# Kernel optimization log

Hardware: AMD Instinct MI355X
Metric: run time of the kernel (lower is better)

The kernel has to match this reference:

```python
import jax, jax.numpy as jnp
import numpy as np

B, T, C = 4, 2048, 1024

def setup_inputs() -> dict:
    key = jax.random.key(0)
    kx, kq, kk, kv = jax.random.split(key, 4)
    s = C ** -0.5  # match nn.Linear init scale roughly
    return {
        "x": jax.random.normal(kx, (B, T, C), dtype=jnp.float32),
        "Wq": jax.random.normal(kq, (C, C), dtype=jnp.float32) * s,
        "Wk": jax.random.normal(kk, (C, C), dtype=jnp.float32) * s,
        "Wv": jax.random.normal(kv, (C, C), dtype=jnp.float32) * s,
    }

def reference(x, Wq, Wk, Wv):
    Bq, Tq, Cq = x.shape
    # nn.Linear: y = x @ W^T (bias=False)
    q = jnp.einsum('btc,dc->btd', x, Wq)
    k = jnp.einsum('btc,dc->btd', x, Wk)
    v = jnp.einsum('btc,dc->btd', x, Wv)
    scale = Cq ** -0.5
    qk = jnp.einsum('btd,bsd->bts', q, k) * scale  # [B, T, T]
    causal = jnp.tril(jnp.ones((Tq, Tq), dtype=bool))
    qk = jnp.where(causal, qk, -jnp.inf)
    attn = jax.nn.softmax(qk, axis=-1)
    out = jnp.einsum('bts,bsd->btd', attn, v)
    return out
```

## Files before the change

### kernel.cpp

```cpp
#include <hip/hip_runtime.h>
#include <hip/hip_fp16.h>


typedef __attribute__((ext_vector_type(8))) _Float16 half8;
typedef __attribute__((ext_vector_type(4))) _Float16 half4;
typedef __attribute__((ext_vector_type(4))) float f32x4;

#define AS1 __attribute__((address_space(1)))
#define AS3 __attribute__((address_space(3)))

__device__ __forceinline__ void gload_lds16(const void* g, void* l) {
    __builtin_amdgcn_global_load_lds((AS1 void*)g, (AS3 void*)l, 16, 0, 0);
}

__device__ __forceinline__ void barrier_np() {
    __asm__ volatile("" ::: "memory");
    __builtin_amdgcn_s_barrier();
    __asm__ volatile("" ::: "memory");
}

template<int TM, int TN, bool SWAP>
__device__ __forceinline__ void gemm_nt_dbuf(
    const _Float16* __restrict__ A, const _Float16* __restrict__ B,
    int lda, int ldb, int k0, int k1,
    _Float16* ldsA, _Float16* ldsB,
    f32x4 acc[TM / 32][TN / 32])
{
    constexpr int FM = TM / 32, FN = TN / 32;
    constexpr int NA = TM / 64, NB = TN / 64;
    constexpr int WAIT_IMM = 0xF70 | (NA + NB);
    const int t    = threadIdx.x;
    const int lane = t & 63;
    const int wm   = (t >> 7) & 1;
    const int wn   = (t >> 6) & 1;
    const int lr   = lane & 15;
    const int lq   = lane >> 4;

    const _Float16* ga[NA]; int loA[NA];
    const _Float16* gb[NB]; int loB[NB];
#pragma unroll
    for (int i = 0; i < NA; ++i) {
        int f = t + 256 * i;
        int r = f >> 2, c = ((f & 3) ^ ((f >> 3) & 3)) * 8;
        ga[i] = A + (size_t)r * lda + c;
        loA[i] = f * 8;
    }
#pragma unroll
    for (int i = 0; i < NB; ++i) {
        int f = t + 256 * i;
        int r = f >> 2, c = ((f & 3) ^ ((f >> 3) & 3)) * 8;
        gb[i] = B + (size_t)r * ldb + c;
        loB[i] = f * 8;
    }

    int offA[FM], offB[FN];
#pragma unroll
    for (int i = 0; i < FM; ++i) {
        int R = wm * (TM / 2) + i * 16 + lr;
        offA[i] = (R * 4 + ((lq ^ (R >> 1)) & 3)) * 8;
    }
#pragma unroll
    for (int i = 0; i < FN; ++i) {
        int R = wn * (TN / 2) + i * 16 + lr;
        offB[i] = (R * 4 + ((lq ^ (R >> 1)) & 3)) * 8;
    }

#pragma unroll
    for (int i = 0; i < NA; ++i) gload_lds16(ga[i] + k0, ldsA + loA[i]);
#pragma unroll
    for (int i = 0; i < NB; ++i) gload_lds16(gb[i] + k0, ldsB + loB[i]);

    int sel = 0;
    for (int k = k0; k < k1; k += 32) {
        const int kp = (k + 32 < k1) ? k + 32 : k;
        _Float16* pA = ldsA + (sel ^ 1) * (TM * 32);
        _Float16* pB = ldsB + (sel ^ 1) * (TN * 32);
#pragma unroll
        for (int i = 0; i < NA; ++i) gload_lds16(ga[i] + kp, pA + loA[i]);
#pragma unroll
        for (int i = 0; i < NB; ++i) gload_lds16(gb[i] + kp, pB + loB[i]);

        __builtin_amdgcn_s_waitcnt(WAIT_IMM);
        barrier_np();

        const _Float16* bufA = ldsA + sel * (TM * 32);
        const _Float16* bufB = ldsB + sel * (TN * 32);
        half8 af[FM], bf[FN];
#pragma unroll
        for (int i = 0; i < FM; ++i) af[i] = *(const half8*)(bufA + offA[i]);
#pragma unroll
        for (int i = 0; i < FN; ++i) bf[i] = *(const half8*)(bufB + offB[i]);
#pragma unroll
        for (int mi = 0; mi < FM; ++mi)
#pragma unroll
            for (int ni = 0; ni < FN; ++ni) {
                if constexpr (SWAP)
                    acc[mi][ni] = __builtin_amdgcn_mfma_f32_16x16x32_f16(
                        bf[ni], af[mi], acc[mi][ni], 0, 0, 0);
                else
                    acc[mi][ni] = __builtin_amdgcn_mfma_f32_16x16x32_f16(
                        af[mi], bf[ni], acc[mi][ni], 0, 0, 0);
            }
        barrier_np();
        sel ^= 1;
    }
}

__global__ __launch_bounds__(256) void f32tof16_k(
    const float* __restrict__ in, _Float16* __restrict__ out, int n)
{
    int i = (blockIdx.x * 256 + threadIdx.x) * 4;
    if (i < n) {
        float4 f = *(const float4*)(in + i);
        half4 h = { (_Float16)f.x, (_Float16)f.y, (_Float16)f.z, (_Float16)f.w };
        *(half4*)(out + i) = h;
    }
}

__global__ __launch_bounds__(256) void wconv_k(
    const float* __restrict__ Wq, const float* __restrict__ Wk,
    const float* __restrict__ Wv, _Float16* __restrict__ out)
{
    const float* src = (blockIdx.y == 0) ? Wq : (blockIdx.y == 1) ? Wk : Wv;
    int i = (blockIdx.x * 256 + threadIdx.x) * 4;
    float4 f = *(const float4*)(src + i);
    half4 h = { (_Float16)f.x, (_Float16)f.y, (_Float16)f.z, (_Float16)f.w };
    *(half4*)(out + (size_t)blockIdx.y * 1024 * 1024 + i) = h;
}

__global__ __launch_bounds__(256) void qkv_gemm_k(
    const _Float16* __restrict__ xh, const _Float16* __restrict__ Wh,
    _Float16* __restrict__ Q, _Float16* __restrict__ K, _Float16* __restrict__ Vt)
{
    __shared__ __align__(16) _Float16 ldsA[2 * 128 * 32];
    __shared__ __align__(16) _Float16 ldsB[2 * 128 * 32];
    const int tileM = blockIdx.x * 128;
    const int tileN = blockIdx.y * 128;
    const int z     = blockIdx.z;
    const _Float16* W = Wh + (size_t)z * 1024 * 1024;

    const int lane = threadIdx.x & 63;
    const int wm = (threadIdx.x >> 7) & 1, wn = (threadIdx.x >> 6) & 1;
    const int lr = lane & 15, lq = lane >> 4;

    if (z == 2) {
        f32x4 acc[4][4] = {};
        gemm_nt_dbuf<128, 128, false>(xh + (size_t)tileM * 1024,
                                      W + (size_t)tileN * 1024,
                                      1024, 1024, 0, 1024, ldsA, ldsB, acc);
#pragma unroll
        for (int mi = 0; mi < 4; ++mi)
#pragma unroll
            for (int ni = 0; ni < 4; ++ni) {
                int m0 = tileM + wm * 64 + mi * 16 + lq * 4;
                int n  = tileN + wn * 64 + ni * 16 + lr;
                int b = m0 >> 11, tt = m0 & 2047;
                half4 h = { (_Float16)acc[mi][ni][0], (_Float16)acc[mi][ni][1],
                            (_Float16)acc[mi][ni][2], (_Float16)acc[mi][ni][3] };
                *(half4*)(Vt + (size_t)b * 2048 * 1024 + (size_t)n * 2048 + tt) = h;
            }
    } else {
        f32x4 acc[4][4] = {};
        gemm_nt_dbuf<128, 128, true>(xh + (size_t)tileM * 1024,
                                     W + (size_t)tileN * 1024,
                                     1024, 1024, 0, 1024, ldsA, ldsB, acc);
        _Float16* O = (z == 0) ? Q : K;
#pragma unroll
        for (int mi = 0; mi < 4; ++mi)
#pragma unroll
            for (int ni = 0; ni < 4; ++ni) {
                int tt = tileM + wm * 64 + mi * 16 + lr;
                int d0 = tileN + wn * 64 + ni * 16 + lq * 4;
                half4 h = { (_Float16)acc[mi][ni][0], (_Float16)acc[mi][ni][1],
                            (_Float16)acc[mi][ni][2], (_Float16)acc[mi][ni][3] };
                *(half4*)(O + (size_t)tt * 1024 + d0) = h;
            }
    }
}

__global__ __launch_bounds__(256) void scores_gemm_k(
    const _Float16* __restrict__ Q, const _Float16* __restrict__ K,
    _Float16* __restrict__ S)
{
    const int ti = blockIdx.x, si = blockIdx.y;
    if (si > ti) return;
    const int tileT = ti * 128, tileS = si * 128, b = blockIdx.z;

    __shared__ __align__(16) _Float16 ldsA[2 * 128 * 32];
    __shared__ __align__(16) _Float16 ldsB[2 * 128 * 32];
    f32x4 acc[4][4] = {};
    gemm_nt_dbuf<128, 128, true>(
        Q + (size_t)b * 2048 * 1024 + (size_t)tileT * 1024,
        K + (size_t)b * 2048 * 1024 + (size_t)tileS * 1024,
        1024, 1024, 0, 1024, ldsA, ldsB, acc);

    const int lane = threadIdx.x & 63;
    const int wm = (threadIdx.x >> 7) & 1, wn = (threadIdx.x >> 6) & 1;
    const int lr = lane & 15, lq = lane >> 4;
    const float scale = 0.03125f;

#pragma unroll
    for (int mi = 0; mi < 4; ++mi)
#pragma unroll
        for (int ni = 0; ni < 4; ++ni) {
            int tt = tileT + wm * 64 + mi * 16 + lr;
            int s0 = tileS + wn * 64 + ni * 16 + lq * 4;
            half4 h;
#pragma unroll
            for (int r = 0; r < 4; ++r)
                h[r] = (s0 + r <= tt) ? (_Float16)(acc[mi][ni][r] * scale)
                                      : (_Float16)0.f;
            *(half4*)(S + ((size_t)b * 2048 + tt) * 2048 + s0) = h;
        }
}

__global__ __launch_bounds__(256) void softmax_k(_Float16* __restrict__ S)
{
    const int w    = threadIdx.x >> 6;
    const int lane = threadIdx.x & 63;
    const int t    = blockIdx.x * 4 + w;
    const int b    = blockIdx.y;
    _Float16* row = S + ((size_t)b * 2048 + t) * 2048;

    float x[32];
    float mx = -1e30f;
#pragma unroll
    for (int j = 0; j < 4; ++j) {
        half8 h = *(const half8*)(row + j * 512 + lane * 8);
#pragma unroll
        for (int e = 0; e < 8; ++e) {
            int s = j * 512 + lane * 8 + e;
            float f = (s <= t) ? (float)h[e] : -1e30f;
            x[j * 8 + e] = f;
            mx = fmaxf(mx, f);
        }
    }
#pragma unroll
    for (int o = 32; o > 0; o >>= 1) mx = fmaxf(mx, __shfl_xor(mx, o));

    float sum = 0.f;
#pragma unroll
    for (int i = 0; i < 32; ++i) {
        float e = __expf(x[i] - mx);
        x[i] = e;
        sum += e;
    }
#pragma unroll
    for (int o = 32; o > 0; o >>= 1) sum += __shfl_xor(sum, o);
    const float inv = 1.0f / sum;

#pragma unroll
    for (int j = 0; j < 4; ++j) {
        half8 p;
#pragma unroll
        for (int e = 0; e < 8; ++e) p[e] = (_Float16)(x[j * 8 + e] * inv);
        *(half8*)(row + j * 512 + lane * 8) = p;
    }
}

__global__ __launch_bounds__(256) void pv_gemm_k(
    const _Float16* __restrict__ P, const _Float16* __restrict__ Vt,
    float* __restrict__ out)
{
    __shared__ __align__(16) _Float16 ldsA[2 * 128 * 32];
    __shared__ __align__(16) _Float16 ldsB[2 * 64 * 32];
    const int tileT = (15 - blockIdx.x) * 128;
    const int tileD = blockIdx.y * 64;
    const int b     = blockIdx.z;
    const int kEnd  = tileT + 128;

    f32x4 acc[4][2] = {};
    gemm_nt_dbuf<128, 64, true>(
        P + ((size_t)b * 2048 + tileT) * 2048,
        Vt + (size_t)b * 1024 * 2048 + (size_t)tileD * 2048,
        2048, 2048, 0, kEnd, ldsA, ldsB, acc);

    const int lane = threadIdx.x & 63;
    const int wm = (threadIdx.x >> 7) & 1, wn = (threadIdx.x >> 6) & 1;
    const int lr = lane & 15, lq = lane >> 4;

#pragma unroll
    for (int mi = 0; mi < 4; ++mi)
#pragma unroll
        for (int ni = 0; ni < 2; ++ni) {
            int tt = tileT + wm * 64 + mi * 16 + lr;
            int d0 = tileD + wn * 32 + ni * 16 + lq * 4;
            *(f32x4*)(out + ((size_t)b * 2048 + tt) * 1024 + d0) = acc[mi][ni];
        }
}

extern "C" void kernel_launch(void* const* d_in, const int* in_sizes, int n_in,
                              void* d_out, int out_size, void* d_ws, size_t ws_size,
                              hipStream_t stream)
{
    const float* x  = (const float*)d_in[0];
    const float* Wq = (const float*)d_in[1];
    const float* Wk = (const float*)d_in[2];
    const float* Wv = (const float*)d_in[3];
    float* out = (float*)d_out;

    char* ws = (char*)d_ws;
    _Float16* xh = (_Float16*)(ws);
    _Float16* Wh = (_Float16*)(ws + (16u << 20));
    _Float16* Qh = (_Float16*)(ws + (22u << 20));
    _Float16* Kh = (_Float16*)(ws + (38u << 20));
    _Float16* Vt = (_Float16*)(ws + (54u << 20));
    _Float16* S  = (_Float16*)(ws + (70u << 20));

    f32tof16_k<<<8192, 256, 0, stream>>>(x, xh, 4 * 2048 * 1024);
    wconv_k<<<dim3(1024, 3), 256, 0, stream>>>(Wq, Wk, Wv, Wh);

    qkv_gemm_k<<<dim3(64, 8, 3), 256, 0, stream>>>(xh, Wh, Qh, Kh, Vt);

    scores_gemm_k<<<dim3(16, 16, 4), 256, 0, stream>>>(Qh, Kh, S);
    softmax_k<<<dim3(512, 4), 256, 0, stream>>>(S);
    pv_gemm_k<<<dim3(16, 16, 4), 256, 0, stream>>>(S, Vt, out);
}
```

Baseline: 284.8 us.

## Replace double-buffered BK=32 GEMM loop with single-buffered BK=64 loop

The shared GEMM core drops the double-buffered K=32 pipeline, where the next tile's global-to-LDS loads overlapped the MFMAs, and uses a single buffer with a K step of 64 and two syncthreads per iteration. The LDS swizzle changes to an 8-chunk XOR pattern to fit the wider rows. This halves the number of loop iterations and barriers, but each iteration now waits for its own loads to land before computing, so load latency is no longer hidden within a block. Whether performance holds depends on occupancy across blocks covering that latency.

```diff
diff --git a/kernel.cpp b/kernel.cpp
--- a/kernel.cpp
+++ b/kernel.cpp
@@ -13,22 +13,15 @@
     __builtin_amdgcn_global_load_lds((AS1 void*)g, (AS3 void*)l, 16, 0, 0);
 }
 
-__device__ __forceinline__ void barrier_np() {
-    __asm__ volatile("" ::: "memory");
-    __builtin_amdgcn_s_barrier();
-    __asm__ volatile("" ::: "memory");
-}
-
 template<int TM, int TN, bool SWAP>
-__device__ __forceinline__ void gemm_nt_dbuf(
+__device__ __forceinline__ void gemm_nt_core(
     const _Float16* __restrict__ A, const _Float16* __restrict__ B,
     int lda, int ldb, int k0, int k1,
     _Float16* ldsA, _Float16* ldsB,
     f32x4 acc[TM / 32][TN / 32])
 {
     constexpr int FM = TM / 32, FN = TN / 32;
-    constexpr int NA = TM / 64, NB = TN / 64;
-    constexpr int WAIT_IMM = 0xF70 | (NA + NB);
+    constexpr int NA = TM / 32, NB = TN / 32;
     const int t    = threadIdx.x;
     const int lane = t & 63;
     const int wm   = (t >> 7) & 1;
@@ -41,68 +34,60 @@
 #pragma unroll
     for (int i = 0; i < NA; ++i) {
         int f = t + 256 * i;
-        int r = f >> 2, c = ((f & 3) ^ ((f >> 3) & 3)) * 8;
-        ga[i] = A + (size_t)r * lda + c;
+        int r = f >> 3, c = (f & 7) ^ ((f >> 3) & 7);
+        ga[i] = A + (size_t)r * lda + c * 8;
         loA[i] = f * 8;
     }
 #pragma unroll
     for (int i = 0; i < NB; ++i) {
         int f = t + 256 * i;
-        int r = f >> 2, c = ((f & 3) ^ ((f >> 3) & 3)) * 8;
-        gb[i] = B + (size_t)r * ldb + c;
+        int r = f >> 3, c = (f & 7) ^ ((f >> 3) & 7);
+        gb[i] = B + (size_t)r * ldb + c * 8;
         loB[i] = f * 8;
     }
 
-    int offA[FM], offB[FN];
-#pragma unroll
-    for (int i = 0; i < FM; ++i) {
-        int R = wm * (TM / 2) + i * 16 + lr;
-        offA[i] = (R * 4 + ((lq ^ (R >> 1)) & 3)) * 8;
-    }
-#pragma unroll
-    for (int i = 0; i < FN; ++i) {
-        int R = wn * (TN / 2) + i * 16 + lr;
-        offB[i] = (R * 4 + ((lq ^ (R >> 1)) & 3)) * 8;
-    }
-
-#pragma unroll
-    for (int i = 0; i < NA; ++i) gload_lds16(ga[i] + k0, ldsA + loA[i]);
-#pragma unroll
-    for (int i = 0; i < NB; ++i) gload_lds16(gb[i] + k0, ldsB + loB[i]);
-
-    int sel = 0;
-    for (int k = k0; k < k1; k += 32) {
-        const int kp = (k + 32 < k1) ? k + 32 : k;
-        _Float16* pA = ldsA + (sel ^ 1) * (TM * 32);
-        _Float16* pB = ldsB + (sel ^ 1) * (TN * 32);
-#pragma unroll
-        for (int i = 0; i < NA; ++i) gload_lds16(ga[i] + kp, pA + loA[i]);
-#pragma unroll
-        for (int i = 0; i < NB; ++i) gload_lds16(gb[i] + kp, pB + loB[i]);
-
-        __builtin_amdgcn_s_waitcnt(WAIT_IMM);
-        barrier_np();
-
-        const _Float16* bufA = ldsA + sel * (TM * 32);
-        const _Float16* bufB = ldsB + sel * (TN * 32);
-        half8 af[FM], bf[FN];
-#pragma unroll
-        for (int i = 0; i < FM; ++i) af[i] = *(const half8*)(bufA + offA[i]);
-#pragma unroll
-        for (int i = 0; i < FN; ++i) bf[i] = *(const half8*)(bufB + offB[i]);
-#pragma unroll
-        for (int mi = 0; mi < FM; ++mi)
-#pragma unroll
-            for (int ni = 0; ni < FN; ++ni) {
-                if constexpr (SWAP)
-                    acc[mi][ni] = __builtin_amdgcn_mfma_f32_16x16x32_f16(
-                        bf[ni], af[mi], acc[mi][ni], 0, 0, 0);
-                else
-                    acc[mi][ni] = __builtin_amdgcn_mfma_f32_16x16x32_f16(
-                        af[mi], bf[ni], acc[mi][ni], 0, 0, 0);
-            }
-        barrier_np();
-        sel ^= 1;
+    int offA[2][FM], offB[2][FN];
+#pragma unroll
+    for (int h = 0; h < 2; ++h) {
+#pragma unroll
+        for (int i = 0; i < FM; ++i) {
+            int R = wm * (TM / 2) + i * 16 + lr;
+            offA[h][i] = (8 * R + ((h * 4 + lq) ^ (R & 7))) * 8;
+        }
+#pragma unroll
+        for (int i = 0; i < FN; ++i) {
+            int R = wn * (TN / 2) + i * 16 + lr;
+            offB[h][i] = (8 * R + ((h * 4 + lq) ^ (R & 7))) * 8;
+        }
+    }
+
+    for (int k = k0; k < k1; k += 64) {
+        __syncthreads();
+#pragma unroll
+        for (int i = 0; i < NA; ++i) gload_lds16(ga[i] + k, ldsA + loA[i]);
+#pragma unroll
+        for (int i = 0; i < NB; ++i) gload_lds16(gb[i] + k, ldsB + loB[i]);
+        __syncthreads();
+
+#pragma unroll
+        for (int h = 0; h < 2; ++h) {
+            half8 af[FM], bf[FN];
+#pragma unroll
+            for (int i = 0; i < FM; ++i) af[i] = *(const half8*)(ldsA + offA[h][i]);
+#pragma unroll
+            for (int i = 0; i < FN; ++i) bf[i] = *(const half8*)(ldsB + offB[h][i]);
+#pragma unroll
+            for (int mi = 0; mi < FM; ++mi)
+#pragma unroll
+                for (int ni = 0; ni < FN; ++ni) {
+                    if constexpr (SWAP)
+                        acc[mi][ni] = __builtin_amdgcn_mfma_f32_16x16x32_f16(
+                            bf[ni], af[mi], acc[mi][ni], 0, 0, 0);
+                    else
+                        acc[mi][ni] = __builtin_amdgcn_mfma_f32_16x16x32_f16(
+                            af[mi], bf[ni], acc[mi][ni], 0, 0, 0);
+                }
+        }
     }
 }
 
@@ -132,8 +117,8 @@
     const _Float16* __restrict__ xh, const _Float16* __restrict__ Wh,
     _Float16* __restrict__ Q, _Float16* __restrict__ K, _Float16* __restrict__ Vt)
 {
-    __shared__ __align__(16) _Float16 ldsA[2 * 128 * 32];
-    __shared__ __align__(16) _Float16 ldsB[2 * 128 * 32];
+    __shared__ __align__(16) _Float16 ldsA[128 * 64];
+    __shared__ __align__(16) _Float16 ldsB[128 * 64];
     const int tileM = blockIdx.x * 128;
     const int tileN = blockIdx.y * 128;
     const int z     = blockIdx.z;
@@ -145,7 +130,7 @@
 
     if (z == 2) {
         f32x4 acc[4][4] = {};
-        gemm_nt_dbuf<128, 128, false>(xh + (size_t)tileM * 1024,
+        gemm_nt_core<128, 128, false>(xh + (size_t)tileM * 1024,
                                       W + (size_t)tileN * 1024,
                                       1024, 1024, 0, 1024, ldsA, ldsB, acc);
 #pragma unroll
@@ -161,7 +146,7 @@
             }
     } else {
         f32x4 acc[4][4] = {};
-        gemm_nt_dbuf<128, 128, true>(xh + (size_t)tileM * 1024,
+        gemm_nt_core<128, 128, true>(xh + (size_t)tileM * 1024,
                                      W + (size_t)tileN * 1024,
                                      1024, 1024, 0, 1024, ldsA, ldsB, acc);
         _Float16* O = (z == 0) ? Q : K;
@@ -186,10 +171,10 @@
     if (si > ti) return;
     const int tileT = ti * 128, tileS = si * 128, b = blockIdx.z;
 
-    __shared__ __align__(16) _Float16 ldsA[2 * 128 * 32];
-    __shared__ __align__(16) _Float16 ldsB[2 * 128 * 32];
+    __shared__ __align__(16) _Float16 ldsA[128 * 64];
+    __shared__ __align__(16) _Float16 ldsB[128 * 64];
     f32x4 acc[4][4] = {};
-    gemm_nt_dbuf<128, 128, true>(
+    gemm_nt_core<128, 128, true>(
         Q + (size_t)b * 2048 * 1024 + (size_t)tileT * 1024,
         K + (size_t)b * 2048 * 1024 + (size_t)tileS * 1024,
         1024, 1024, 0, 1024, ldsA, ldsB, acc);
@@ -262,15 +247,15 @@
     const _Float16* __restrict__ P, const _Float16* __restrict__ Vt,
     float* __restrict__ out)
 {
-    __shared__ __align__(16) _Float16 ldsA[2 * 128 * 32];
-    __shared__ __align__(16) _Float16 ldsB[2 * 64 * 32];
+    __shared__ __align__(16) _Float16 ldsA[128 * 64];
+    __shared__ __align__(16) _Float16 ldsB[64 * 64];
     const int tileT = (15 - blockIdx.x) * 128;
     const int tileD = blockIdx.y * 64;
     const int b     = blockIdx.z;
     const int kEnd  = tileT + 128;
 
     f32x4 acc[4][2] = {};
-    gemm_nt_dbuf<128, 64, true>(
+    gemm_nt_core<128, 64, true>(
         P + ((size_t)b * 2048 + tileT) * 2048,
         Vt + (size_t)b * 1024 * 2048 + (size_t)tileD * 2048,
         2048, 2048, 0, kEnd, ldsA, ldsB, acc);
```

New measurement: 262.8 us. -7.7%, faster.
